# Optimization experiments

Measured on AMD Instinct MI355X. Metric: run time of the kernel, lower is better.

Reference implementation:

```python
import jax, jax.numpy as jnp
import numpy as np

C = 1.0          # curvature
TOP_K = 5
LAMBDA_H = 0.01
TAU = 0.1        # forward default
NEG_SAMPLES = 20 # forward default
EPS = 1e-9
B, D = 4096, 64


def _to_ball(v):
    # map gaussian vectors strictly inside the unit Poincare ball
    return 0.8 * v / (1.0 + jnp.linalg.norm(v, axis=-1, keepdims=True))


def setup_inputs() -> dict:
    key = jax.random.key(0)
    ka, kt = jax.random.split(key)
    audio = _to_ball(jax.random.normal(ka, (B, D), dtype=jnp.float32))
    text = _to_ball(jax.random.normal(kt, (B, D), dtype=jnp.float32))
    return {"audio_embeds": audio, "text_embeds": text}


def _pairwise_poincare(x, y, c=C):
    # ||x-y||^2 via gemm instead of materializing [N,N,D] diff tensor
    x_sq = jnp.sum(x * x, axis=-1, keepdims=True)          # [N,1]
    y_sq = jnp.sum(y * y, axis=-1, keepdims=True).T        # [1,M]
    diff_sq = jnp.maximum(x_sq + y_sq - 2.0 * (x @ y.T), 0.0)
    x_cl = jnp.minimum(x_sq, 1.0 - EPS)
    y_cl = jnp.minimum(y_sq, 1.0 - EPS)
    denom = jnp.maximum((1.0 - x_cl) * (1.0 - y_cl), EPS)
    z = jnp.maximum(1.0 + 2.0 * diff_sq / denom, 1.0 + EPS)
    return jnp.arccosh(z) / jnp.sqrt(jnp.asarray(c, x.dtype))


def _topk_triplet(embeds, key):
    n = embeds.shape[0]
    dist = _pairwise_poincare(embeds, embeds)
    dist = dist.at[jnp.arange(n), jnp.arange(n)].set(jnp.inf)  # fill_diagonal_(inf)
    k = min(TOP_K, n - 1)
    neg_pos, pos_idx = jax.lax.top_k(-dist, k)                 # k smallest distances
    pos_term = jax.scipy.special.logsumexp(neg_pos / TAU, axis=1)  # logsumexp(-pos_dist/tau)
    # mask out top-k positives (diagonal stays in pool, holding +inf -> exp(-inf)=0)
    mask = jnp.ones((n, n), bool).at[jnp.arange(n)[:, None], pos_idx].set(False)
    # stable argsort: mask-True columns first, in original column order -> matches dist[i][mask[i]]
    order = jnp.argsort(jnp.where(mask, 0, 1), axis=1)
    pool = jnp.take_along_axis(dist, order[:, : n - k], axis=1)    # [n, n-k]
    samp = jax.random.randint(key, (n, NEG_SAMPLES), 0, n - k)
    neg_vals = jnp.take_along_axis(pool, samp, axis=1)             # [n, NEG_SAMPLES]
    neg_term = jax.scipy.special.logsumexp(-neg_vals / TAU, axis=1)
    return jnp.mean(neg_term - pos_term)  # mean of -(pos_term - neg_term)


def reference(audio_embeds, text_embeds):
    # HyperbolicLayeredLoss.forward returns lambda_h * (text_h + audio_h);
    # the cross-modal loss is computed but NOT added to the returned total in the source.
    key_text = jax.random.key(1)
    key_audio = jax.random.key(2)
    loss_text_h = _topk_triplet(text_embeds, key_text)
    loss_audio_h = _topk_triplet(audio_embeds, key_audio)
    return LAMBDA_H * (loss_text_h + loss_audio_h)
```

## Files before the change

kernel.cpp:

```cpp
#include <hip/hip_runtime.h>
#include <stdint.h>

constexpr int N = 4096;
constexpr int DIM = 64;
constexpr int TOPK = 5;
constexpr int NEGS = 20;
constexpr float TAU_ = 0.1f;
constexpr uint32_t SPAN = 4091u;
constexpr uint32_t MULT = 2309u;

constexpr int CQ = 256;
constexpr int NSLAB = N / CQ;
constexpr int NT = CQ / 16;
constexpr int RPB = 64;
constexpr int YSTRIDE = 136;
constexpr int NSAMP = 4;
constexpr int CAP = 256;

typedef __attribute__((ext_vector_type(8))) short bf16x8;
typedef __attribute__((ext_vector_type(4))) float f32x4;

struct U2 { uint32_t a, b; };

constexpr U2 tf20(uint32_t k0, uint32_t k1, uint32_t x0, uint32_t x1) {
  const uint32_t k2 = k0 ^ k1 ^ 0x1BD11BDAu;
  x0 += k0; x1 += k1;
#define TF_C(r) { x0 += x1; x1 = (x1 << (r)) | (x1 >> (32 - (r))); x1 ^= x0; }
  TF_C(13) TF_C(15) TF_C(26) TF_C(6)
  x0 += k1; x1 += k2 + 1u;
  TF_C(17) TF_C(29) TF_C(16) TF_C(24)
  x0 += k2; x1 += k0 + 2u;
  TF_C(13) TF_C(15) TF_C(26) TF_C(6)
  x0 += k0; x1 += k1 + 3u;
  TF_C(17) TF_C(29) TF_C(16) TF_C(24)
  x0 += k1; x1 += k2 + 4u;
  TF_C(13) TF_C(15) TF_C(26) TF_C(6)
  x0 += k2; x1 += k0 + 5u;
#undef TF_C
  return {x0, x1};
}
constexpr U2 KT1 = tf20(0u, 1u, 0u, 0u);
constexpr U2 KT2 = tf20(0u, 1u, 0u, 1u);
constexpr U2 KA1 = tf20(0u, 2u, 0u, 0u);
constexpr U2 KA2 = tf20(0u, 2u, 0u, 1u);

__device__ __forceinline__ uint32_t rotl32(uint32_t v, int d) {
  return (v << d) | (v >> (32 - d));
}
__device__ __forceinline__ void threefry(uint32_t k0, uint32_t k1,
                                         uint32_t& x0, uint32_t& x1) {
  const uint32_t k2 = k0 ^ k1 ^ 0x1BD11BDAu;
  x0 += k0; x1 += k1;
#define TF_R(r) { x0 += x1; x1 = rotl32(x1, r); x1 ^= x0; }
  TF_R(13) TF_R(15) TF_R(26) TF_R(6)
  x0 += k1; x1 += k2 + 1u;
  TF_R(17) TF_R(29) TF_R(16) TF_R(24)
  x0 += k2; x1 += k0 + 2u;
  TF_R(13) TF_R(15) TF_R(26) TF_R(6)
  x0 += k0; x1 += k1 + 3u;
  TF_R(17) TF_R(29) TF_R(16) TF_R(24)
  x0 += k1; x1 += k2 + 4u;
  TF_R(13) TF_R(15) TF_R(26) TF_R(6)
  x0 += k2; x1 += k0 + 5u;
#undef TF_R
}

__device__ __forceinline__ uint32_t sample_idx(U2 K1, U2 K2, uint32_t f) {
  uint32_t h0 = 0u, h1 = f; threefry(K1.a, K1.b, h0, h1);
  const uint32_t hi = h0 ^ h1;
  uint32_t l0 = 0u, l1 = f; threefry(K2.a, K2.b, l0, l1);
  const uint32_t lo = l0 ^ l1;
  return ((hi % SPAN) * MULT + (lo % SPAN)) % SPAN;
}

__device__ __forceinline__ float acosh_dev(float z) {
  return logf(z + sqrtf((z - 1.0f) * (z + 1.0f)));
}
__device__ __forceinline__ uint16_t f2bf(float f) {
  const uint32_t u = __float_as_uint(f);
  return (uint16_t)((u + 0x7FFFu + ((u >> 16) & 1u)) >> 16);
}
__device__ __forceinline__ float bf2f(uint16_t h) {
  return __uint_as_float((uint32_t)h << 16);
}

__global__ __launch_bounds__(64) void k_pre(const float* __restrict__ Xa,
                                            const float* __restrict__ Xt,
                                            uint16_t* __restrict__ Xs,
                                            float* __restrict__ ysq,
                                            float* __restrict__ inv,
                                            uint32_t* __restrict__ cnt) {
  const int m = blockIdx.y;
  const float* __restrict__ X = (m == 0) ? Xt : Xa;
  const int i = blockIdx.x * 64 + threadIdx.x;
  const float* xr = X + (size_t)i * DIM;

  uint32_t hb[DIM / 2], lb[DIM / 2];
  float s = 0.0f;
#pragma unroll
  for (int u = 0; u < DIM / 4; ++u) {
    const float4 v = *(const float4*)(xr + 4 * u);
    s = fmaf(v.x, v.x, s); s = fmaf(v.y, v.y, s);
    s = fmaf(v.z, v.z, s); s = fmaf(v.w, v.w, s);
    const uint16_t h0 = f2bf(v.x), h1 = f2bf(v.y), h2 = f2bf(v.z), h3 = f2bf(v.w);
    const uint16_t l0 = f2bf(v.x - bf2f(h0)), l1 = f2bf(v.y - bf2f(h1));
    const uint16_t l2 = f2bf(v.z - bf2f(h2)), l3 = f2bf(v.w - bf2f(h3));
    hb[2 * u]     = (uint32_t)h0 | ((uint32_t)h1 << 16);
    hb[2 * u + 1] = (uint32_t)h2 | ((uint32_t)h3 << 16);
    lb[2 * u]     = (uint32_t)l0 | ((uint32_t)l1 << 16);
    lb[2 * u + 1] = (uint32_t)l2 | ((uint32_t)l3 << 16);
  }
  uint32_t* dst = (uint32_t*)(Xs + (size_t)(m * N + i) * 128);
#pragma unroll
  for (int w = 0; w < 8; ++w) {
    uint4 qh = { hb[4 * w], hb[4 * w + 1], hb[4 * w + 2], hb[4 * w + 3] };
    ((uint4*)dst)[w] = qh;
  }
#pragma unroll
  for (int w = 0; w < 8; ++w) {
    uint4 ql = { lb[4 * w], lb[4 * w + 1], lb[4 * w + 2], lb[4 * w + 3] };
    ((uint4*)dst)[8 + w] = ql;
  }
  ysq[m * N + i] = s;
  inv[m * N + i] = 1.0f / (1.0f - fminf(s, 1.0f));
  cnt[m * N + i] = 0u;
}


__global__ __launch_bounds__(256) void k_zb4(
    const uint16_t* __restrict__ Xs, const float* __restrict__ ysq,
    const float* __restrict__ inv, float* __restrict__ zb5) {
  const int rb = (int)blockIdx.x;
  const int qs = (int)blockIdx.y;
  const int m = (int)blockIdx.z;
  const int j0q = (qs * 4 + 1) * CQ;

  const int tid = (int)threadIdx.x;
  const int wid = tid >> 6;
  const int l = tid & 63;
  const int i0w = rb * RPB + wid * 16;
  const int mN = m * N;
  const uint16_t* __restrict__ Xm = Xs + (size_t)m * N * 128;
  const int lc = l & 15;
  const int lk = l >> 4;
  const int lk4 = lk * 4;
  const int lk8 = lk * 8;
  const int sr = tid >> 4;
  const int sc8 = (tid & 15) * 8;
  const int gi = i0w + lc;
  const int dso = sr * YSTRIDE + sc8;

  __shared__ __align__(16) unsigned char smem[4 * 16 * YSTRIDE * 2 + 2048];
  uint16_t* ybuf = (uint16_t*)smem;
  float* sq_s = (float*)(smem + 4 * 16 * YSTRIDE * 2);
  float* iv_s = sq_s + CQ;

  bf16x8 xf[2][2];
#pragma unroll
  for (int c = 0; c < 2; ++c)
#pragma unroll
    for (int h = 0; h < 2; ++h)
      xf[c][h] = *(const bf16x8*)(Xm + (size_t)gi * 128 + h * 64 + c * 32 + lk8);

  const float xsq_i = ysq[mN + gi];

  float t5f[TOPK];
#pragma unroll
  for (int t = 0; t < TOPK; ++t) t5f[t] = __uint_as_float(0x7F800000u);

  const f32x4 zz = {0.0f, 0.0f, 0.0f, 0.0f};
  const float INF_ = __uint_as_float(0x7F800000u);
  const uint16_t* gsrc = Xm + (size_t)(j0q + sr) * 128 + sc8;

#define GLOAD2(A, B, T)                                                        \
  { A = *(const uint4*)(gsrc + (size_t)(T) * 2048);                            \
    B = *(const uint4*)(gsrc + (size_t)((T) + 1) * 2048); }
#define DSW2(A, B, PB)                                                         \
  { *(uint4*)(ybuf + (size_t)((PB) * 2) * (16 * YSTRIDE) + dso) = A;           \
    *(uint4*)(ybuf + (size_t)((PB) * 2 + 1) * (16 * YSTRIDE) + dso) = B; }

#define PZB(T, BUF)                                                            \
  {                                                                            \
    const uint16_t* yp = (BUF) + lc * YSTRIDE + lk8;                           \
    const bf16x8 Y0 = *(const bf16x8*)(yp);                                    \
    const bf16x8 Y1 = *(const bf16x8*)(yp + 32);                               \
    const bf16x8 Y2 = *(const bf16x8*)(yp + 64);                               \
    const bf16x8 Y3 = *(const bf16x8*)(yp + 96);                               \
    f32x4 acc;        \
    acc = __builtin_amdgcn_mfma_f32_16x16x32_bf16(Y0, xf[0][0], zz, 0, 0, 0);  \
    acc = __builtin_amdgcn_mfma_f32_16x16x32_bf16(Y1, xf[1][0], acc, 0, 0, 0); \
    acc = __builtin_amdgcn_mfma_f32_16x16x32_bf16(Y2, xf[0][0], acc, 0, 0, 0); \
    acc = __builtin_amdgcn_mfma_f32_16x16x32_bf16(Y3, xf[1][0], acc, 0, 0, 0); \
    acc = __builtin_amdgcn_mfma_f32_16x16x32_bf16(Y0, xf[0][1], acc, 0, 0, 0); \
    acc = __builtin_amdgcn_mfma_f32_16x16x32_bf16(Y1, xf[1][1], acc, 0, 0, 0); \
    const float4 sq4 = *(const float4*)&sq_s[(T) * 16 + lk4];                  \
    const float4 iv4 = *(const float4*)&iv_s[(T) * 16 + lk4];                  \
    const int jb = j0q + (T) * 16;                                             \
    float st[4];                                                               \
    _Pragma("unroll") for (int p = 0; p < 4; ++p) {                            \
      const float yc = (p == 0) ? sq4.x : (p == 1) ? sq4.y                     \
                      : (p == 2) ? sq4.z : sq4.w;                              \
      const float ic = (p == 0) ? iv4.x : (p == 1) ? iv4.y                     \
                      : (p == 2) ? iv4.z : iv4.w;                              \
      const float d = fmaf(-2.0f, acc[p], xsq_i + yc);                         \
      st[p] = fmaxf(d, 0.0f) * ic;      \
    }                                                                          \
    if (jb == i0w) {                                                           \
      _Pragma("unroll") for (int p = 0; p < 4; ++p)                            \
        if (gi == jb + lk4 + p) st[p] = INF_;                                  \
    }                                                                          \
    _Pragma("unroll") for (int p = 0; p < 4; ++p) {                            \
      float v = st[p];              \
      _Pragma("unroll") for (int t = 0; t < TOPK; ++t) {                       \
        const float mn = fminf(t5f[t], v);                                     \
        v = fmaxf(t5f[t], v);                                                  \
        t5f[t] = mn;                                                           \
      }                                                                        \
    }                                                                          \
  }

  uint4 Ra0, Ra1, Rb0, Rb1;
  if (tid < 64)
    *(float4*)&sq_s[tid * 4] = *(const float4*)&ysq[mN + j0q + tid * 4];
  else if (tid < 128)
    *(float4*)&iv_s[(tid - 64) * 4] =
        *(const float4*)&inv[mN + j0q + (tid - 64) * 4];
  GLOAD2(Ra0, Ra1, 0)
  GLOAD2(Rb0, Rb1, 2)
  DSW2(Ra0, Ra1, 0)

#pragma unroll 1
  for (int p = 0; p < NT / 2; ++p) {
    __syncthreads();
    if (p + 2 < NT / 2) {
      if ((p & 1) == 0) GLOAD2(Ra0, Ra1, (p + 2) * 2)
      else              GLOAD2(Rb0, Rb1, (p + 2) * 2)
    }
    if (p + 1 < NT / 2) {
      if ((p & 1) == 0) DSW2(Rb0, Rb1, 1)
      else              DSW2(Ra0, Ra1, 0)
    }
    PZB(2 * p,     ybuf + (size_t)((p & 1) * 2) * (16 * YSTRIDE))
    PZB(2 * p + 1, ybuf + (size_t)((p & 1) * 2 + 1) * (16 * YSTRIDE))
  }
#undef PZB

  __syncthreads();
  float* mb = (float*)smem;
#pragma unroll
  for (int t = 0; t < TOPK; ++t)
    mb[((size_t)(wid * 16) + lc) * 21 + lk * TOPK + t] = t5f[t];
  __syncthreads();

  if (l < 16) {
    float cur[TOPK];
#pragma unroll
    for (int t = 0; t < TOPK; ++t) cur[t] = mb[((size_t)(wid * 16) + l) * 21 + t];
    for (int c = 1; c < 4; ++c) {
      for (int t = 0; t < TOPK; ++t) {
        float v = mb[((size_t)(wid * 16) + l) * 21 + c * TOPK + t];
        if (v >= cur[TOPK - 1]) break;
#pragma unroll
        for (int u = 0; u < TOPK; ++u) {
          const float mn = fminf(cur[u], v);
          v = fmaxf(cur[u], v);
          cur[u] = mn;
        }
      }
    }
#pragma unroll
    for (int t = 0; t < TOPK; ++t)
      zb5[((size_t)(m * NSAMP + qs) * N + i0w + l) * TOPK + t] = cur[t];
  }
}

__global__ __launch_bounds__(256) void k_scan(
    const uint16_t* __restrict__ Xs, const float* __restrict__ ysq,
    const float* __restrict__ inv, const float* __restrict__ zb5,
    uint32_t* __restrict__ cnt, uint64_t* __restrict__ rowlist) {
  const int rb = (int)blockIdx.x;
  const int qq = (int)blockIdx.y;
  const int m = (int)blockIdx.z;
  const int j0q = qq * CQ;

  const int tid = (int)threadIdx.x;
  const int wid = tid >> 6;
  const int l = tid & 63;
  const int i0b = rb * RPB;
  const int i0w = i0b + wid * 16;
  const int mN = m * N;
  const uint16_t* __restrict__ Xm = Xs + (size_t)m * N * 128;
  const int lc = l & 15;
  const int lk = l >> 4;
  const int lk4 = lk * 4;
  const int lk8 = lk * 8;
  const int sr = tid >> 4;
  const int sc8 = (tid & 15) * 8;
  const int gi = i0w + lc;
  const int dso = sr * YSTRIDE + sc8;

  __shared__ __align__(16) unsigned char smem[4 * 16 * YSTRIDE * 2 + 2048];
  __shared__ float bs_s[RPB];
  uint16_t* ybuf = (uint16_t*)smem;
  float* sq_s = (float*)(smem + 4 * 16 * YSTRIDE * 2);
  float* iv_s = sq_s + CQ;

  bf16x8 xf[2][2];
#pragma unroll
  for (int c = 0; c < 2; ++c)
#pragma unroll
    for (int h = 0; h < 2; ++h)
      xf[c][h] = *(const bf16x8*)(Xm + (size_t)gi * 128 + h * 64 + c * 32 + lk8);

  const float xsq_i = ysq[mN + gi];

  const f32x4 zz = {0.0f, 0.0f, 0.0f, 0.0f};
  const float INF_ = __uint_as_float(0x7F800000u);
  const uint16_t* gsrc = Xm + (size_t)(j0q + sr) * 128 + sc8;

#define PSCAN(T, BUF)                                                          \
  {                                                                            \
    const uint16_t* yp = (BUF) + lc * YSTRIDE + lk8;                           \
    const bf16x8 Y0 = *(const bf16x8*)(yp);                                    \
    const bf16x8 Y1 = *(const bf16x8*)(yp + 32);                               \
    const bf16x8 Y2 = *(const bf16x8*)(yp + 64);                               \
    const bf16x8 Y3 = *(const bf16x8*)(yp + 96);                               \
    f32x4 acc;                        \
    acc = __builtin_amdgcn_mfma_f32_16x16x32_bf16(Y0, xf[0][0], zz, 0, 0, 0);  \
    acc = __builtin_amdgcn_mfma_f32_16x16x32_bf16(Y1, xf[1][0], acc, 0, 0, 0); \
    acc = __builtin_amdgcn_mfma_f32_16x16x32_bf16(Y2, xf[0][0], acc, 0, 0, 0); \
    acc = __builtin_amdgcn_mfma_f32_16x16x32_bf16(Y3, xf[1][0], acc, 0, 0, 0); \
    acc = __builtin_amdgcn_mfma_f32_16x16x32_bf16(Y0, xf[0][1], acc, 0, 0, 0); \
    acc = __builtin_amdgcn_mfma_f32_16x16x32_bf16(Y1, xf[1][1], acc, 0, 0, 0); \
    const float4 sq4 = *(const float4*)&sq_s[(T) * 16 + lk4];                  \
    const float4 iv4 = *(const float4*)&iv_s[(T) * 16 + lk4];                  \
    const int jb = j0q + (T) * 16;                                             \
    float st[4];                                                               \
    _Pragma("unroll") for (int p = 0; p < 4; ++p) {                            \
      const float yc = (p == 0) ? sq4.x : (p == 1) ? sq4.y                     \
                      : (p == 2) ? sq4.z : sq4.w;                              \
      const float ic = (p == 0) ? iv4.x : (p == 1) ? iv4.y                     \
                      : (p == 2) ? iv4.z : iv4.w;                              \
      const float d = fmaf(-2.0f, acc[p], xsq_i + yc);                         \
      st[p] = fmaxf(d, 0.0f) * ic;                                             \
    }                                                                          \
    if (jb == i0w) {                                                           \
      _Pragma("unroll") for (int p = 0; p < 4; ++p)                            \
        if (gi == jb + lk4 + p) st[p] = INF_;                                  \
    }                                                                          \
    const float sm = fminf(fminf(st[0], st[1]), fminf(st[2], st[3]));          \
    if (sm <= bz) {                                                            \
      _Pragma("unroll") for (int p = 0; p < 4; ++p) {                          \
        if (st[p] <= bz) {                                                     \
          const uint64_t key = ((uint64_t)__float_as_uint(st[p]) << 32) |      \
                               (uint32_t)(jb + lk4 + p);                       \
          const uint32_t slot = atomicAdd(&cnt[mN + gi], 1u);                  \
          if (slot < (uint32_t)CAP)                                            \
            rowlist[(size_t)(mN + gi) * CAP + slot] = key;                     \
        }                                                                      \
      }                                                                        \
    }                                                                          \
  }

  uint4 Ra0, Ra1, Rb0, Rb1;
  if (tid < 64) {
    const int row = i0b + tid;
    float cur[TOPK];
#pragma unroll
    for (int t = 0; t < TOPK; ++t)
      cur[t] = zb5[((size_t)(m * NSAMP) * N + row) * TOPK + t];
    for (int q = 1; q < NSAMP; ++q) {
      for (int t = 0; t < TOPK; ++t) {
        float v = zb5[((size_t)(m * NSAMP + q) * N + row) * TOPK + t];
        if (v >= cur[TOPK - 1]) break;
#pragma unroll
        for (int u = 0; u < TOPK; ++u) {
          const float mn = fminf(cur[u], v);
          v = fmaxf(cur[u], v);
          cur[u] = mn;
        }
      }
    }
    bs_s[tid] = cur[TOPK - 1];
    *(float4*)&sq_s[tid * 4] = *(const float4*)&ysq[mN + j0q + tid * 4];
  } else if (tid < 128) {
    *(float4*)&iv_s[(tid - 64) * 4] =
        *(const float4*)&inv[mN + j0q + (tid - 64) * 4];
  }
  GLOAD2(Ra0, Ra1, 0)
  GLOAD2(Rb0, Rb1, 2)
  DSW2(Ra0, Ra1, 0)
  __syncthreads();
  const float bz = bs_s[wid * 16 + lc];

#pragma unroll 1
  for (int p = 0; p < NT / 2; ++p) {
    if (p) __syncthreads();
    if (p + 2 < NT / 2) {
      if ((p & 1) == 0) GLOAD2(Ra0, Ra1, (p + 2) * 2)
      else              GLOAD2(Rb0, Rb1, (p + 2) * 2)
    }
    if (p + 1 < NT / 2) {
      if ((p & 1) == 0) DSW2(Rb0, Rb1, 1)
      else              DSW2(Ra0, Ra1, 0)
    }
    PSCAN(2 * p,     ybuf + (size_t)((p & 1) * 2) * (16 * YSTRIDE))
    PSCAN(2 * p + 1, ybuf + (size_t)((p & 1) * 2 + 1) * (16 * YSTRIDE))
  }
#undef PSCAN
#undef GLOAD2
#undef DSW2
}

__global__ __launch_bounds__(64) void k_neg(const float* __restrict__ Xa,
                                            const float* __restrict__ Xt,
                                            const float* __restrict__ ysq,
                                            const float* __restrict__ inv,
                                            const uint32_t* __restrict__ cnt,
                                            const uint64_t* __restrict__ rowlist,
                                            float* __restrict__ rowres) {
  const int m = blockIdx.y;
  const int i = blockIdx.x;
  const float* __restrict__ X = (m == 0) ? Xt : Xa;
  const U2 K1 = (m == 0) ? KT1 : KA1;
  const U2 K2 = (m == 0) ? KT2 : KA2;
  const int lane = threadIdx.x;

  __shared__ float4 xi4[DIM / 4];
  __shared__ float posv[TOPK];
  if (lane < DIM / 4) xi4[lane] = ((const float4*)(X + (size_t)i * DIM))[lane];
  __syncthreads();

  const uint64_t SENT = ((uint64_t)0x7F800000u << 32) | 0xFFFFFFFFu;
  uint64_t cur[TOPK];
#pragma unroll
  for (int t = 0; t < TOPK; ++t) cur[t] = SENT;
  {
    const uint32_t c_ = min(cnt[m * N + i], (uint32_t)CAP);
    for (uint32_t sv = 0; sv < c_; ++sv) {
      uint64_t key = rowlist[(size_t)(m * N + i) * CAP + sv];
      if (key < cur[TOPK - 1]) {
#pragma unroll
        for (int u = 0; u < TOPK; ++u) {
          const uint64_t cv = cur[u];
          if (key < cv) { cur[u] = key; key = cv; }
        }
      }
    }
  }

  const float ysq_i = ysq[m * N + i];
  const float inv_i = inv[m * N + i];

  if (lane >= 32 && lane < 32 + TOPK) {
    const int t = lane - 32;
    const uint32_t c = (uint32_t)(cur[t] & 0xffffffffu);
    const float4* xc = (const float4*)(X + (size_t)c * DIM);
    float dot = 0.0f;
#pragma unroll
    for (int k = 0; k < DIM / 4; ++k) {
      const float4 a = xi4[k];
      const float4 b = xc[k];
      dot = fmaf(a.x, b.x, dot); dot = fmaf(a.y, b.y, dot);
      dot = fmaf(a.z, b.z, dot); dot = fmaf(a.w, b.w, dot);
    }
    const float diff = fmaxf(ysq_i + ysq[m * N + c] - 2.0f * dot, 0.0f);
    const float z = 1.0f + 2.0f * diff * inv_i * inv[m * N + c];
    posv[t] = -acosh_dev(z) / TAU_;
  }

  uint32_t pidx[TOPK];
#pragma unroll
  for (int t = 0; t < TOPK; ++t) pidx[t] = (uint32_t)(cur[t] & 0xffffffffu);

#define CSWAP(a, b)                                                           \
  { const uint32_t mn = pidx[a] < pidx[b] ? pidx[a] : pidx[b];                \
    const uint32_t mx = pidx[a] < pidx[b] ? pidx[b] : pidx[a];                \
    pidx[a] = mn; pidx[b] = mx; }
  CSWAP(0, 1) CSWAP(3, 4) CSWAP(2, 4) CSWAP(2, 3) CSWAP(1, 4)
  CSWAP(0, 3) CSWAP(0, 2) CSWAP(1, 3) CSWAP(1, 2)
#undef CSWAP

  float v = -1e30f;
  if (lane < NEGS) {
    const uint32_t f = (uint32_t)i * (uint32_t)NEGS + (uint32_t)lane;
    uint32_t c = sample_idx(K1, K2, f);
#pragma unroll
    for (int t = 0; t < TOPK; ++t) c += (c >= pidx[t]) ? 1u : 0u;
    if (c != (uint32_t)i) {
      const float4* xc = (const float4*)(X + (size_t)c * DIM);
      float dot = 0.0f;
#pragma unroll
      for (int k = 0; k < DIM / 4; ++k) {
        const float4 a = xi4[k];
        const float4 b = xc[k];
        dot = fmaf(a.x, b.x, dot); dot = fmaf(a.y, b.y, dot);
        dot = fmaf(a.z, b.z, dot); dot = fmaf(a.w, b.w, dot);
      }
      const float diff = fmaxf(ysq_i + ysq[m * N + c] - 2.0f * dot, 0.0f);
      const float z = 1.0f + 2.0f * diff * inv_i * inv[m * N + c];
      v = -acosh_dev(z) / TAU_;
    }
  }

  __syncthreads();

  float vmax = v;
#pragma unroll
  for (int o = 32; o > 0; o >>= 1) vmax = fmaxf(vmax, __shfl_xor(vmax, o, 64));
  float e = expf(v - vmax);
  float ss = e;
#pragma unroll
  for (int o = 32; o > 0; o >>= 1) ss += __shfl_xor(ss, o, 64);

  if (lane == 0) {
    float vm = -1e30f;
#pragma unroll
    for (int t = 0; t < TOPK; ++t) vm = fmaxf(vm, posv[t]);
    float ps = 0.0f;
#pragma unroll
    for (int t = 0; t < TOPK; ++t) ps += expf(posv[t] - vm);
    const float pos = vm + logf(ps);
    rowres[m * N + i] = (vmax + logf(ss)) - pos;
  }
}

__global__ __launch_bounds__(256) void k_reduce(const float* __restrict__ rowres,
                                                float* __restrict__ out) {
  __shared__ double sh[256];
  double s = 0.0;
  for (int idx = threadIdx.x; idx < 2 * N; idx += 256) s += (double)rowres[idx];
  sh[threadIdx.x] = s;
  __syncthreads();
  for (int o = 128; o > 0; o >>= 1) {
    if (threadIdx.x < o) sh[threadIdx.x] += sh[threadIdx.x + o];
    __syncthreads();
  }
  if (threadIdx.x == 0) out[0] = (float)(0.01 * (sh[0] / (double)N));
}

extern "C" void kernel_launch(void* const* d_in, const int* in_sizes, int n_in,
                              void* d_out, int out_size, void* d_ws,
                              size_t ws_size, hipStream_t stream) {
  const float* Xa = (const float*)d_in[0];
  const float* Xt = (const float*)d_in[1];
  float* out = (float*)d_out;

  float* ysq = (float*)d_ws;
  float* inv = ysq + 2 * N;
  float* rowres = inv + 2 * N;
  uint32_t* cnt = (uint32_t*)(rowres + 2 * N);
  float* zb5 = (float*)(cnt + 2 * N);
  uint64_t* rowlist = (uint64_t*)(zb5 + (size_t)2 * NSAMP * N * TOPK);
  uint16_t* Xs = (uint16_t*)(rowlist + (size_t)2 * N * CAP);

  k_pre<<<dim3(N / 64, 2), 64, 0, stream>>>(Xa, Xt, Xs, ysq, inv, cnt);
  k_zb4<<<dim3(N / RPB, NSAMP, 2), 256, 0, stream>>>(Xs, ysq, inv, zb5);
  k_scan<<<dim3(N / RPB, NSLAB, 2), 256, 0, stream>>>(Xs, ysq, inv, zb5, cnt,
                                                      rowlist);
  k_neg<<<dim3(N, 2), 64, 0, stream>>>(Xa, Xt, ysq, inv, cnt, rowlist, rowres);
  k_reduce<<<1, 256, 0, stream>>>(rowres, out);
}
```

Measured before the change: 105.4 us.

## Merge threshold pass into single selection scan with local running top-k filter

Removes the k_zb4 pre-pass that sampled slabs to build a top-5 distance bound. The scan kernel now keeps a per-lane running top-5 and emits candidates whenever they beat its current fifth-best value. Two MFMA chains are interleaved across the even and odd tiles. The candidate cap grows to 2048 because early slabs have weak bounds, so k_neg now reduces the candidate list in parallel across 64 lanes and merges through shared memory. This saves one full pass and a launch, but adds more atomics and global writes for candidates and a larger workspace.

```diff
diff --git a/kernel.cpp b/kernel.cpp
--- a/kernel.cpp
+++ b/kernel.cpp
@@ -14,8 +14,7 @@
 constexpr int NT = CQ / 16;
 constexpr int RPB = 64;
 constexpr int YSTRIDE = 136;
-constexpr int NSAMP = 4;
-constexpr int CAP = 256;
+constexpr int CAP = 2048;
 
 typedef __attribute__((ext_vector_type(8))) short bf16x8;
 typedef __attribute__((ext_vector_type(4))) float f32x4;
@@ -126,14 +125,14 @@
   cnt[m * N + i] = 0u;
 }
 
-
-__global__ __launch_bounds__(256) void k_zb4(
+__global__ __launch_bounds__(256) void k_sel(
     const uint16_t* __restrict__ Xs, const float* __restrict__ ysq,
-    const float* __restrict__ inv, float* __restrict__ zb5) {
+    const float* __restrict__ inv, uint32_t* __restrict__ cnt,
+    uint64_t* __restrict__ rowlist) {
   const int rb = (int)blockIdx.x;
-  const int qs = (int)blockIdx.y;
+  const int qq = (int)blockIdx.y;
   const int m = (int)blockIdx.z;
-  const int j0q = (qs * 4 + 1) * CQ;
+  const int j0q = qq * CQ;
 
   const int tid = (int)threadIdx.x;
   const int wid = tid >> 6;
@@ -179,20 +178,8 @@
   { *(uint4*)(ybuf + (size_t)((PB) * 2) * (16 * YSTRIDE) + dso) = A;           \
     *(uint4*)(ybuf + (size_t)((PB) * 2 + 1) * (16 * YSTRIDE) + dso) = B; }
 
-#define PZB(T, BUF)                                                            \
+#define EPI(T, ACC)                                                            \
   {                                                                            \
-    const uint16_t* yp = (BUF) + lc * YSTRIDE + lk8;                           \
-    const bf16x8 Y0 = *(const bf16x8*)(yp);                                    \
-    const bf16x8 Y1 = *(const bf16x8*)(yp + 32);                               \
-    const bf16x8 Y2 = *(const bf16x8*)(yp + 64);                               \
-    const bf16x8 Y3 = *(const bf16x8*)(yp + 96);                               \
-    f32x4 acc;        \
-    acc = __builtin_amdgcn_mfma_f32_16x16x32_bf16(Y0, xf[0][0], zz, 0, 0, 0);  \
-    acc = __builtin_amdgcn_mfma_f32_16x16x32_bf16(Y1, xf[1][0], acc, 0, 0, 0); \
-    acc = __builtin_amdgcn_mfma_f32_16x16x32_bf16(Y2, xf[0][0], acc, 0, 0, 0); \
-    acc = __builtin_amdgcn_mfma_f32_16x16x32_bf16(Y3, xf[1][0], acc, 0, 0, 0); \
-    acc = __builtin_amdgcn_mfma_f32_16x16x32_bf16(Y0, xf[0][1], acc, 0, 0, 0); \
-    acc = __builtin_amdgcn_mfma_f32_16x16x32_bf16(Y1, xf[1][1], acc, 0, 0, 0); \
     const float4 sq4 = *(const float4*)&sq_s[(T) * 16 + lk4];                  \
     const float4 iv4 = *(const float4*)&iv_s[(T) * 16 + lk4];                  \
     const int jb = j0q + (T) * 16;                                             \
@@ -202,19 +189,29 @@
                       : (p == 2) ? sq4.z : sq4.w;                              \
       const float ic = (p == 0) ? iv4.x : (p == 1) ? iv4.y                     \
                       : (p == 2) ? iv4.z : iv4.w;                              \
-      const float d = fmaf(-2.0f, acc[p], xsq_i + yc);                         \
+      const float d = fmaf(-2.0f, ACC[p], xsq_i + yc);                         \
       st[p] = fmaxf(d, 0.0f) * ic;      \
     }                                                                          \
-    if (jb == i0w) {                                                           \
+    if (jb == i0w) {                           \
       _Pragma("unroll") for (int p = 0; p < 4; ++p)                            \
         if (gi == jb + lk4 + p) st[p] = INF_;                                  \
     }                                                                          \
-    _Pragma("unroll") for (int p = 0; p < 4; ++p) {                            \
-      float v = st[p];              \
-      _Pragma("unroll") for (int t = 0; t < TOPK; ++t) {                       \
-        const float mn = fminf(t5f[t], v);                                     \
-        v = fmaxf(t5f[t], v);                                                  \
-        t5f[t] = mn;                                                           \
+    const float sm = fminf(fminf(st[0], st[1]), fminf(st[2], st[3]));          \
+    if (sm <= t5f[TOPK - 1]) {                                                 \
+      _Pragma("unroll") for (int p = 0; p < 4; ++p) {                          \
+        if (st[p] <= t5f[TOPK - 1]) {        \
+          const uint64_t key = ((uint64_t)__float_as_uint(st[p]) << 32) |      \
+                               (uint32_t)(jb + lk4 + p);                       \
+          const uint32_t slot = atomicAdd(&cnt[mN + gi], 1u);                  \
+          if (slot < (uint32_t)CAP)                                            \
+            rowlist[(size_t)(mN + gi) * CAP + slot] = key;                     \
+          float v = st[p];                       \
+          _Pragma("unroll") for (int t = 0; t < TOPK; ++t) {                   \
+            const float mn = fminf(t5f[t], v);                                 \
+            v = fmaxf(t5f[t], v);                                              \
+            t5f[t] = mn;                                                       \
+          }                                                                    \
+        }                                                                      \
       }                                                                        \
     }                                                                          \
   }
@@ -240,174 +237,35 @@
       if ((p & 1) == 0) DSW2(Rb0, Rb1, 1)
       else              DSW2(Ra0, Ra1, 0)
     }
-    PZB(2 * p,     ybuf + (size_t)((p & 1) * 2) * (16 * YSTRIDE))
-    PZB(2 * p + 1, ybuf + (size_t)((p & 1) * 2 + 1) * (16 * YSTRIDE))
-  }
-#undef PZB
-
-  __syncthreads();
-  float* mb = (float*)smem;
-#pragma unroll
-  for (int t = 0; t < TOPK; ++t)
-    mb[((size_t)(wid * 16) + lc) * 21 + lk * TOPK + t] = t5f[t];
-  __syncthreads();
-
-  if (l < 16) {
-    float cur[TOPK];
-#pragma unroll
-    for (int t = 0; t < TOPK; ++t) cur[t] = mb[((size_t)(wid * 16) + l) * 21 + t];
-    for (int c = 1; c < 4; ++c) {
-      for (int t = 0; t < TOPK; ++t) {
-        float v = mb[((size_t)(wid * 16) + l) * 21 + c * TOPK + t];
-        if (v >= cur[TOPK - 1]) break;
-#pragma unroll
-        for (int u = 0; u < TOPK; ++u) {
-          const float mn = fminf(cur[u], v);
-          v = fmaxf(cur[u], v);
-          cur[u] = mn;
-        }
-      }
-    }
-#pragma unroll
-    for (int t = 0; t < TOPK; ++t)
-      zb5[((size_t)(m * NSAMP + qs) * N + i0w + l) * TOPK + t] = cur[t];
-  }
-}
-
-__global__ __launch_bounds__(256) void k_scan(
-    const uint16_t* __restrict__ Xs, const float* __restrict__ ysq,
-    const float* __restrict__ inv, const float* __restrict__ zb5,
-    uint32_t* __restrict__ cnt, uint64_t* __restrict__ rowlist) {
-  const int rb = (int)blockIdx.x;
-  const int qq = (int)blockIdx.y;
-  const int m = (int)blockIdx.z;
-  const int j0q = qq * CQ;
-
-  const int tid = (int)threadIdx.x;
-  const int wid = tid >> 6;
-  const int l = tid & 63;
-  const int i0b = rb * RPB;
-  const int i0w = i0b + wid * 16;
-  const int mN = m * N;
-  const uint16_t* __restrict__ Xm = Xs + (size_t)m * N * 128;
-  const int lc = l & 15;
-  const int lk = l >> 4;
-  const int lk4 = lk * 4;
-  const int lk8 = lk * 8;
-  const int sr = tid >> 4;
-  const int sc8 = (tid & 15) * 8;
-  const int gi = i0w + lc;
-  const int dso = sr * YSTRIDE + sc8;
-
-  __shared__ __align__(16) unsigned char smem[4 * 16 * YSTRIDE * 2 + 2048];
-  __shared__ float bs_s[RPB];
-  uint16_t* ybuf = (uint16_t*)smem;
-  float* sq_s = (float*)(smem + 4 * 16 * YSTRIDE * 2);
-  float* iv_s = sq_s + CQ;
-
-  bf16x8 xf[2][2];
-#pragma unroll
-  for (int c = 0; c < 2; ++c)
-#pragma unroll
-    for (int h = 0; h < 2; ++h)
-      xf[c][h] = *(const bf16x8*)(Xm + (size_t)gi * 128 + h * 64 + c * 32 + lk8);
-
-  const float xsq_i = ysq[mN + gi];
-
-  const f32x4 zz = {0.0f, 0.0f, 0.0f, 0.0f};
-  const float INF_ = __uint_as_float(0x7F800000u);
-  const uint16_t* gsrc = Xm + (size_t)(j0q + sr) * 128 + sc8;
-
-#define PSCAN(T, BUF)                                                          \
-  {                                                                            \
-    const uint16_t* yp = (BUF) + lc * YSTRIDE + lk8;                           \
-    const bf16x8 Y0 = *(const bf16x8*)(yp);                                    \
-    const bf16x8 Y1 = *(const bf16x8*)(yp + 32);                               \
-    const bf16x8 Y2 = *(const bf16x8*)(yp + 64);                               \
-    const bf16x8 Y3 = *(const bf16x8*)(yp + 96);                               \
-    f32x4 acc;                        \
-    acc = __builtin_amdgcn_mfma_f32_16x16x32_bf16(Y0, xf[0][0], zz, 0, 0, 0);  \
-    acc = __builtin_amdgcn_mfma_f32_16x16x32_bf16(Y1, xf[1][0], acc, 0, 0, 0); \
-    acc = __builtin_amdgcn_mfma_f32_16x16x32_bf16(Y2, xf[0][0], acc, 0, 0, 0); \
-    acc = __builtin_amdgcn_mfma_f32_16x16x32_bf16(Y3, xf[1][0], acc, 0, 0, 0); \
-    acc = __builtin_amdgcn_mfma_f32_16x16x32_bf16(Y0, xf[0][1], acc, 0, 0, 0); \
-    acc = __builtin_amdgcn_mfma_f32_16x16x32_bf16(Y1, xf[1][1], acc, 0, 0, 0); \
-    const float4 sq4 = *(const float4*)&sq_s[(T) * 16 + lk4];                  \
-    const float4 iv4 = *(const float4*)&iv_s[(T) * 16 + lk4];                  \
-    const int jb = j0q + (T) * 16;                                             \
-    float st[4];                                                               \
-    _Pragma("unroll") for (int p = 0; p < 4; ++p) {                            \
-      const float yc = (p == 0) ? sq4.x : (p == 1) ? sq4.y                     \
-                      : (p == 2) ? sq4.z : sq4.w;                              \
-      const float ic = (p == 0) ? iv4.x : (p == 1) ? iv4.y                     \
-                      : (p == 2) ? iv4.z : iv4.w;                              \
-      const float d = fmaf(-2.0f, acc[p], xsq_i + yc);                         \
-      st[p] = fmaxf(d, 0.0f) * ic;                                             \
-    }                                                                          \
-    if (jb == i0w) {                                                           \
-      _Pragma("unroll") for (int p = 0; p < 4; ++p)                            \
-        if (gi == jb + lk4 + p) st[p] = INF_;                                  \
-    }                                                                          \
-    const float sm = fminf(fminf(st[0], st[1]), fminf(st[2], st[3]));          \
-    if (sm <= bz) {                                                            \
-      _Pragma("unroll") for (int p = 0; p < 4; ++p) {                          \
-        if (st[p] <= bz) {                                                     \
-          const uint64_t key = ((uint64_t)__float_as_uint(st[p]) << 32) |      \
-                               (uint32_t)(jb + lk4 + p);                       \
-          const uint32_t slot = atomicAdd(&cnt[mN + gi], 1u);                  \
-          if (slot < (uint32_t)CAP)                                            \
-            rowlist[(size_t)(mN + gi) * CAP + slot] = key;                     \
-        }                                                                      \
-      }                                                                        \
-    }                                                                          \
-  }
-
-  uint4 Ra0, Ra1, Rb0, Rb1;
-  if (tid < 64) {
-    const int row = i0b + tid;
-    float cur[TOPK];
-#pragma unroll
-    for (int t = 0; t < TOPK; ++t)
-      cur[t] = zb5[((size_t)(m * NSAMP) * N + row) * TOPK + t];
-    for (int q = 1; q < NSAMP; ++q) {
-      for (int t = 0; t < TOPK; ++t) {
-        float v = zb5[((size_t)(m * NSAMP + q) * N + row) * TOPK + t];
-        if (v >= cur[TOPK - 1]) break;
-#pragma unroll
-        for (int u = 0; u < TOPK; ++u) {
-          const float mn = fminf(cur[u], v);
-          v = fmaxf(cur[u], v);
-          cur[u] = mn;
-        }
-      }
-    }
-    bs_s[tid] = cur[TOPK - 1];
-    *(float4*)&sq_s[tid * 4] = *(const float4*)&ysq[mN + j0q + tid * 4];
-  } else if (tid < 128) {
-    *(float4*)&iv_s[(tid - 64) * 4] =
-        *(const float4*)&inv[mN + j0q + (tid - 64) * 4];
-  }
-  GLOAD2(Ra0, Ra1, 0)
-  GLOAD2(Rb0, Rb1, 2)
-  DSW2(Ra0, Ra1, 0)
-  __syncthreads();
-  const float bz = bs_s[wid * 16 + lc];
-
-#pragma unroll 1
-  for (int p = 0; p < NT / 2; ++p) {
-    if (p) __syncthreads();
-    if (p + 2 < NT / 2) {
-      if ((p & 1) == 0) GLOAD2(Ra0, Ra1, (p + 2) * 2)
-      else              GLOAD2(Rb0, Rb1, (p + 2) * 2)
-    }
-    if (p + 1 < NT / 2) {
-      if ((p & 1) == 0) DSW2(Rb0, Rb1, 1)
-      else              DSW2(Ra0, Ra1, 0)
-    }
-    PSCAN(2 * p,     ybuf + (size_t)((p & 1) * 2) * (16 * YSTRIDE))
-    PSCAN(2 * p + 1, ybuf + (size_t)((p & 1) * 2 + 1) * (16 * YSTRIDE))
-  }
-#undef PSCAN
+    const uint16_t* ypE =
+        ybuf + (size_t)((p & 1) * 2) * (16 * YSTRIDE) + lc * YSTRIDE + lk8;
+    const uint16_t* ypO =
+        ybuf + (size_t)((p & 1) * 2 + 1) * (16 * YSTRIDE) + lc * YSTRIDE + lk8;
+    const bf16x8 E0 = *(const bf16x8*)(ypE);
+    const bf16x8 E1 = *(const bf16x8*)(ypE + 32);
+    const bf16x8 E2 = *(const bf16x8*)(ypE + 64);
+    const bf16x8 E3 = *(const bf16x8*)(ypE + 96);
+    const bf16x8 O0 = *(const bf16x8*)(ypO);
+    const bf16x8 O1 = *(const bf16x8*)(ypO + 32);
+    const bf16x8 O2 = *(const bf16x8*)(ypO + 64);
+    const bf16x8 O3 = *(const bf16x8*)(ypO + 96);
+    f32x4 aE, aO;
+    aE = __builtin_amdgcn_mfma_f32_16x16x32_bf16(E0, xf[0][0], zz, 0, 0, 0);
+    aO = __builtin_amdgcn_mfma_f32_16x16x32_bf16(O0, xf[0][0], zz, 0, 0, 0);
+    aE = __builtin_amdgcn_mfma_f32_16x16x32_bf16(E1, xf[1][0], aE, 0, 0, 0);
+    aO = __builtin_amdgcn_mfma_f32_16x16x32_bf16(O1, xf[1][0], aO, 0, 0, 0);
+    aE = __builtin_amdgcn_mfma_f32_16x16x32_bf16(E2, xf[0][0], aE, 0, 0, 0);
+    aO = __builtin_amdgcn_mfma_f32_16x16x32_bf16(O2, xf[0][0], aO, 0, 0, 0);
+    aE = __builtin_amdgcn_mfma_f32_16x16x32_bf16(E3, xf[1][0], aE, 0, 0, 0);
+    aO = __builtin_amdgcn_mfma_f32_16x16x32_bf16(O3, xf[1][0], aO, 0, 0, 0);
+    aE = __builtin_amdgcn_mfma_f32_16x16x32_bf16(E0, xf[0][1], aE, 0, 0, 0);
+    aO = __builtin_amdgcn_mfma_f32_16x16x32_bf16(O0, xf[0][1], aO, 0, 0, 0);
+    aE = __builtin_amdgcn_mfma_f32_16x16x32_bf16(E1, xf[1][1], aE, 0, 0, 0);
+    aO = __builtin_amdgcn_mfma_f32_16x16x32_bf16(O1, xf[1][1], aO, 0, 0, 0);
+    EPI(2 * p, aE)
+    EPI(2 * p + 1, aO)
+  }
+#undef EPI
 #undef GLOAD2
 #undef DSW2
 }
@@ -428,8 +286,8 @@
 
   __shared__ float4 xi4[DIM / 4];
   __shared__ float posv[TOPK];
+  __shared__ uint64_t mbuf[64][TOPK + 1];
   if (lane < DIM / 4) xi4[lane] = ((const float4*)(X + (size_t)i * DIM))[lane];
-  __syncthreads();
 
   const uint64_t SENT = ((uint64_t)0x7F800000u << 32) | 0xFFFFFFFFu;
   uint64_t cur[TOPK];
@@ -437,8 +295,9 @@
   for (int t = 0; t < TOPK; ++t) cur[t] = SENT;
   {
     const uint32_t c_ = min(cnt[m * N + i], (uint32_t)CAP);
-    for (uint32_t sv = 0; sv < c_; ++sv) {
-      uint64_t key = rowlist[(size_t)(m * N + i) * CAP + sv];
+    const uint64_t* rl = rowlist + (size_t)(m * N + i) * CAP;
+    for (uint32_t sv = (uint32_t)lane; sv < c_; sv += 64u) {
+      uint64_t key = rl[sv];
       if (key < cur[TOPK - 1]) {
 #pragma unroll
         for (int u = 0; u < TOPK; ++u) {
@@ -448,6 +307,30 @@
       }
     }
   }
+#pragma unroll
+  for (int t = 0; t < TOPK; ++t) mbuf[lane][t] = cur[t];
+  __syncthreads();
+  if (lane == 0) {
+    uint64_t fin[TOPK];
+#pragma unroll
+    for (int t = 0; t < TOPK; ++t) fin[t] = mbuf[0][t];
+    for (int c = 1; c < 64; ++c) {
+      for (int t = 0; t < TOPK; ++t) {
+        uint64_t key = mbuf[c][t];
+        if (key >= fin[TOPK - 1]) break;
+#pragma unroll
+        for (int u = 0; u < TOPK; ++u) {
+          const uint64_t cv = fin[u];
+          if (key < cv) { fin[u] = key; key = cv; }
+        }
+      }
+    }
+#pragma unroll
+    for (int t = 0; t < TOPK; ++t) mbuf[0][t] = fin[t];
+  }
+  __syncthreads();
+#pragma unroll
+  for (int t = 0; t < TOPK; ++t) cur[t] = mbuf[0][t];
 
   const float ysq_i = ysq[m * N + i];
   const float inv_i = inv[m * N + i];
@@ -550,14 +433,12 @@
   float* inv = ysq + 2 * N;
   float* rowres = inv + 2 * N;
   uint32_t* cnt = (uint32_t*)(rowres + 2 * N);
-  float* zb5 = (float*)(cnt + 2 * N);
-  uint64_t* rowlist = (uint64_t*)(zb5 + (size_t)2 * NSAMP * N * TOPK);
+  uint64_t* rowlist = (uint64_t*)(cnt + 2 * N);
   uint16_t* Xs = (uint16_t*)(rowlist + (size_t)2 * N * CAP);
 
   k_pre<<<dim3(N / 64, 2), 64, 0, stream>>>(Xa, Xt, Xs, ysq, inv, cnt);
-  k_zb4<<<dim3(N / RPB, NSAMP, 2), 256, 0, stream>>>(Xs, ysq, inv, zb5);
-  k_scan<<<dim3(N / RPB, NSLAB, 2), 256, 0, stream>>>(Xs, ysq, inv, zb5, cnt,
-                                                      rowlist);
+  k_sel<<<dim3(N / RPB, NSLAB, 2), 256, 0, stream>>>(Xs, ysq, inv, cnt,
+                                                     rowlist);
   k_neg<<<dim3(N, 2), 64, 0, stream>>>(Xa, Xt, ysq, inv, cnt, rowlist, rowres);
   k_reduce<<<1, 256, 0, stream>>>(rowres, out);
 }
```

New measurement: 389.0 us. +269.2%, slower.

## Compute exact partial top-5 over bound region and skip it in scan

Applied to the files above, without the earlier changes.

The bound kernel now covers 1024 columns per row block (16 sub-blocks of 64 columns, each near the row's own quarter) and keeps exact top-5 keys that pack distance with index, instead of float-only bounds from 4 sampled slabs. The scan kernel then skips those 4 slabs (12 slabs instead of 16), filters candidates with a strict 64-bit key bound, and k_neg seeds its top-5 from the merged partial results. The scan does less work and emits fewer atomics, at the cost of more bound blocks, larger partial buffers, and a 16-way merge in both k_scan and k_neg.

```diff
diff --git a/kernel.cpp b/kernel.cpp
--- a/kernel.cpp
+++ b/kernel.cpp
@@ -14,7 +14,8 @@
 constexpr int NT = CQ / 16;
 constexpr int RPB = 64;
 constexpr int YSTRIDE = 136;
-constexpr int NSAMP = 4;
+constexpr int NQB = 4;
+constexpr int NBL = 16;
 constexpr int CAP = 256;
 
 typedef __attribute__((ext_vector_type(8))) short bf16x8;
@@ -126,14 +127,16 @@
   cnt[m * N + i] = 0u;
 }
 
-
-__global__ __launch_bounds__(256) void k_zb4(
+__global__ __launch_bounds__(256) void k_bound(
     const uint16_t* __restrict__ Xs, const float* __restrict__ ysq,
-    const float* __restrict__ inv, float* __restrict__ zb5) {
+    const float* __restrict__ inv, uint64_t* __restrict__ partial) {
   const int rb = (int)blockIdx.x;
-  const int qs = (int)blockIdx.y;
+  const int qy = (int)blockIdx.y;
   const int m = (int)blockIdx.z;
-  const int j0q = (qs * 4 + 1) * CQ;
+  const int qr = rb >> 4;
+  const int qs = qy >> 2;
+  const int tq = qy & 3;
+  const int j0 = (qr * NQB + qs) * CQ + tq * 64;
 
   const int tid = (int)threadIdx.x;
   const int wid = tid >> 6;
@@ -150,10 +153,10 @@
   const int gi = i0w + lc;
   const int dso = sr * YSTRIDE + sc8;
 
-  __shared__ __align__(16) unsigned char smem[4 * 16 * YSTRIDE * 2 + 2048];
+  __shared__ __align__(16) unsigned char smem[4 * 16 * YSTRIDE * 2 + 512];
   uint16_t* ybuf = (uint16_t*)smem;
   float* sq_s = (float*)(smem + 4 * 16 * YSTRIDE * 2);
-  float* iv_s = sq_s + CQ;
+  float* iv_s = sq_s + 64;
 
   bf16x8 xf[2][2];
 #pragma unroll
@@ -164,124 +167,122 @@
 
   const float xsq_i = ysq[mN + gi];
 
-  float t5f[TOPK];
-#pragma unroll
-  for (int t = 0; t < TOPK; ++t) t5f[t] = __uint_as_float(0x7F800000u);
+  const uint64_t SENT = ((uint64_t)0x7F800000u << 32) | 0xFFFFFFFFu;
+  uint64_t t5[TOPK];
+#pragma unroll
+  for (int t = 0; t < TOPK; ++t) t5[t] = SENT;
+  float s5 = __uint_as_float(0x7F800000u);
 
   const f32x4 zz = {0.0f, 0.0f, 0.0f, 0.0f};
   const float INF_ = __uint_as_float(0x7F800000u);
-  const uint16_t* gsrc = Xm + (size_t)(j0q + sr) * 128 + sc8;
-
-#define GLOAD2(A, B, T)                                                        \
-  { A = *(const uint4*)(gsrc + (size_t)(T) * 2048);                            \
-    B = *(const uint4*)(gsrc + (size_t)((T) + 1) * 2048); }
-#define DSW2(A, B, PB)                                                         \
-  { *(uint4*)(ybuf + (size_t)((PB) * 2) * (16 * YSTRIDE) + dso) = A;           \
-    *(uint4*)(ybuf + (size_t)((PB) * 2 + 1) * (16 * YSTRIDE) + dso) = B; }
-
-#define PZB(T, BUF)                                                            \
-  {                                                                            \
-    const uint16_t* yp = (BUF) + lc * YSTRIDE + lk8;                           \
-    const bf16x8 Y0 = *(const bf16x8*)(yp);                                    \
-    const bf16x8 Y1 = *(const bf16x8*)(yp + 32);                               \
-    const bf16x8 Y2 = *(const bf16x8*)(yp + 64);                               \
-    const bf16x8 Y3 = *(const bf16x8*)(yp + 96);                               \
-    f32x4 acc;        \
-    acc = __builtin_amdgcn_mfma_f32_16x16x32_bf16(Y0, xf[0][0], zz, 0, 0, 0);  \
-    acc = __builtin_amdgcn_mfma_f32_16x16x32_bf16(Y1, xf[1][0], acc, 0, 0, 0); \
-    acc = __builtin_amdgcn_mfma_f32_16x16x32_bf16(Y2, xf[0][0], acc, 0, 0, 0); \
-    acc = __builtin_amdgcn_mfma_f32_16x16x32_bf16(Y3, xf[1][0], acc, 0, 0, 0); \
-    acc = __builtin_amdgcn_mfma_f32_16x16x32_bf16(Y0, xf[0][1], acc, 0, 0, 0); \
-    acc = __builtin_amdgcn_mfma_f32_16x16x32_bf16(Y1, xf[1][1], acc, 0, 0, 0); \
-    const float4 sq4 = *(const float4*)&sq_s[(T) * 16 + lk4];                  \
-    const float4 iv4 = *(const float4*)&iv_s[(T) * 16 + lk4];                  \
-    const int jb = j0q + (T) * 16;                                             \
-    float st[4];                                                               \
-    _Pragma("unroll") for (int p = 0; p < 4; ++p) {                            \
-      const float yc = (p == 0) ? sq4.x : (p == 1) ? sq4.y                     \
-                      : (p == 2) ? sq4.z : sq4.w;                              \
-      const float ic = (p == 0) ? iv4.x : (p == 1) ? iv4.y                     \
-                      : (p == 2) ? iv4.z : iv4.w;                              \
-      const float d = fmaf(-2.0f, acc[p], xsq_i + yc);                         \
-      st[p] = fmaxf(d, 0.0f) * ic;      \
-    }                                                                          \
-    if (jb == i0w) {                                                           \
-      _Pragma("unroll") for (int p = 0; p < 4; ++p)                            \
-        if (gi == jb + lk4 + p) st[p] = INF_;                                  \
-    }                                                                          \
-    _Pragma("unroll") for (int p = 0; p < 4; ++p) {                            \
-      float v = st[p];              \
-      _Pragma("unroll") for (int t = 0; t < TOPK; ++t) {                       \
-        const float mn = fminf(t5f[t], v);                                     \
-        v = fmaxf(t5f[t], v);                                                  \
-        t5f[t] = mn;                                                           \
-      }                                                                        \
-    }                                                                          \
-  }
-
-  uint4 Ra0, Ra1, Rb0, Rb1;
-  if (tid < 64)
-    *(float4*)&sq_s[tid * 4] = *(const float4*)&ysq[mN + j0q + tid * 4];
-  else if (tid < 128)
-    *(float4*)&iv_s[(tid - 64) * 4] =
-        *(const float4*)&inv[mN + j0q + (tid - 64) * 4];
-  GLOAD2(Ra0, Ra1, 0)
-  GLOAD2(Rb0, Rb1, 2)
-  DSW2(Ra0, Ra1, 0)
-
-#pragma unroll 1
-  for (int p = 0; p < NT / 2; ++p) {
+
+  {
+    const uint16_t* gsrc = Xm + (size_t)(j0 + sr) * 128 + sc8;
+    const uint4 r0 = *(const uint4*)(gsrc);
+    const uint4 r1 = *(const uint4*)(gsrc + 2048);
+    const uint4 r2 = *(const uint4*)(gsrc + 4096);
+    const uint4 r3 = *(const uint4*)(gsrc + 6144);
+    if (tid < 16)
+      *(float4*)&sq_s[tid * 4] = *(const float4*)&ysq[mN + j0 + tid * 4];
+    else if (tid < 32)
+      *(float4*)&iv_s[(tid - 16) * 4] =
+          *(const float4*)&inv[mN + j0 + (tid - 16) * 4];
+    *(uint4*)(ybuf + (size_t)0 * 16 * YSTRIDE + dso) = r0;
+    *(uint4*)(ybuf + (size_t)1 * 16 * YSTRIDE + dso) = r1;
+    *(uint4*)(ybuf + (size_t)2 * 16 * YSTRIDE + dso) = r2;
+    *(uint4*)(ybuf + (size_t)3 * 16 * YSTRIDE + dso) = r3;
     __syncthreads();
-    if (p + 2 < NT / 2) {
-      if ((p & 1) == 0) GLOAD2(Ra0, Ra1, (p + 2) * 2)
-      else              GLOAD2(Rb0, Rb1, (p + 2) * 2)
-    }
-    if (p + 1 < NT / 2) {
-      if ((p & 1) == 0) DSW2(Rb0, Rb1, 1)
-      else              DSW2(Ra0, Ra1, 0)
-    }
-    PZB(2 * p,     ybuf + (size_t)((p & 1) * 2) * (16 * YSTRIDE))
-    PZB(2 * p + 1, ybuf + (size_t)((p & 1) * 2 + 1) * (16 * YSTRIDE))
-  }
-#undef PZB
+  }
+
+#pragma unroll
+  for (int T = 0; T < 4; ++T) {
+    const uint16_t* yp =
+        ybuf + (size_t)T * 16 * YSTRIDE + lc * YSTRIDE + lk8;
+    const bf16x8 Y0 = *(const bf16x8*)(yp);
+    const bf16x8 Y1 = *(const bf16x8*)(yp + 32);
+    const bf16x8 Y2 = *(const bf16x8*)(yp + 64);
+    const bf16x8 Y3 = *(const bf16x8*)(yp + 96);
+    f32x4 acc;
+    acc = __builtin_amdgcn_mfma_f32_16x16x32_bf16(Y0, xf[0][0], zz, 0, 0, 0);
+    acc = __builtin_amdgcn_mfma_f32_16x16x32_bf16(Y1, xf[1][0], acc, 0, 0, 0);
+    acc = __builtin_amdgcn_mfma_f32_16x16x32_bf16(Y2, xf[0][0], acc, 0, 0, 0);
+    acc = __builtin_amdgcn_mfma_f32_16x16x32_bf16(Y3, xf[1][0], acc, 0, 0, 0);
+    acc = __builtin_amdgcn_mfma_f32_16x16x32_bf16(Y0, xf[0][1], acc, 0, 0, 0);
+    acc = __builtin_amdgcn_mfma_f32_16x16x32_bf16(Y1, xf[1][1], acc, 0, 0, 0);
+    const float4 sq4 = *(const float4*)&sq_s[T * 16 + lk4];
+    const float4 iv4 = *(const float4*)&iv_s[T * 16 + lk4];
+    const int jb = j0 + T * 16;
+    float st[4];
+#pragma unroll
+    for (int p = 0; p < 4; ++p) {
+      const float yc = (p == 0) ? sq4.x : (p == 1) ? sq4.y
+                      : (p == 2) ? sq4.z : sq4.w;
+      const float ic = (p == 0) ? iv4.x : (p == 1) ? iv4.y
+                      : (p == 2) ? iv4.z : iv4.w;
+      const float d = fmaf(-2.0f, acc[p], xsq_i + yc);
+      st[p] = fmaxf(d, 0.0f) * ic;
+    }
+    if (jb == i0w) {
+#pragma unroll
+      for (int p = 0; p < 4; ++p)
+        if (gi == jb + lk4 + p) st[p] = INF_;
+    }
+    const float sm = fminf(fminf(st[0], st[1]), fminf(st[2], st[3]));
+    if (sm <= s5) {
+#pragma unroll
+      for (int p = 0; p < 4; ++p) {
+        uint64_t key = ((uint64_t)__float_as_uint(st[p]) << 32) |
+                       (uint32_t)(jb + lk4 + p);
+        if (key < t5[TOPK - 1]) {
+#pragma unroll
+          for (int tt = 0; tt < TOPK; ++tt) {
+            const uint64_t cv = t5[tt];
+            if (key < cv) { t5[tt] = key; key = cv; }
+          }
+        }
+      }
+      s5 = __uint_as_float((uint32_t)(t5[TOPK - 1] >> 32));
+    }
+  }
 
   __syncthreads();
-  float* mb = (float*)smem;
+  uint64_t* mb = (uint64_t*)smem;
 #pragma unroll
   for (int t = 0; t < TOPK; ++t)
-    mb[((size_t)(wid * 16) + lc) * 21 + lk * TOPK + t] = t5f[t];
+    mb[((size_t)(wid * 16) + lc) * 21 + lk * TOPK + t] = t5[t];
   __syncthreads();
 
   if (l < 16) {
-    float cur[TOPK];
+    uint64_t cur[TOPK];
 #pragma unroll
     for (int t = 0; t < TOPK; ++t) cur[t] = mb[((size_t)(wid * 16) + l) * 21 + t];
     for (int c = 1; c < 4; ++c) {
       for (int t = 0; t < TOPK; ++t) {
-        float v = mb[((size_t)(wid * 16) + l) * 21 + c * TOPK + t];
-        if (v >= cur[TOPK - 1]) break;
+        uint64_t key = mb[((size_t)(wid * 16) + l) * 21 + c * TOPK + t];
+        if (key >= cur[TOPK - 1]) break;
 #pragma unroll
         for (int u = 0; u < TOPK; ++u) {
-          const float mn = fminf(cur[u], v);
-          v = fmaxf(cur[u], v);
-          cur[u] = mn;
+          const uint64_t cv = cur[u];
+          if (key < cv) { cur[u] = key; key = cv; }
         }
       }
     }
 #pragma unroll
     for (int t = 0; t < TOPK; ++t)
-      zb5[((size_t)(m * NSAMP + qs) * N + i0w + l) * TOPK + t] = cur[t];
+      partial[((size_t)(m * NBL + qy) * N + i0w + l) * TOPK + t] = cur[t];
   }
 }
 
 __global__ __launch_bounds__(256) void k_scan(
     const uint16_t* __restrict__ Xs, const float* __restrict__ ysq,
-    const float* __restrict__ inv, const float* __restrict__ zb5,
+    const float* __restrict__ inv, const uint64_t* __restrict__ partial,
     uint32_t* __restrict__ cnt, uint64_t* __restrict__ rowlist) {
   const int rb = (int)blockIdx.x;
-  const int qq = (int)blockIdx.y;
+  const int s = (int)blockIdx.y;
   const int m = (int)blockIdx.z;
-  const int j0q = qq * CQ;
+  const int qr = rb >> 4;
+  const int gs = (s < qr * NQB) ? s : s + NQB;
+  const int j0q = gs * CQ;
 
   const int tid = (int)threadIdx.x;
   const int wid = tid >> 6;
@@ -300,7 +301,7 @@
   const int dso = sr * YSTRIDE + sc8;
 
   __shared__ __align__(16) unsigned char smem[4 * 16 * YSTRIDE * 2 + 2048];
-  __shared__ float bs_s[RPB];
+  __shared__ uint64_t bnd_s[RPB];
   uint16_t* ybuf = (uint16_t*)smem;
   float* sq_s = (float*)(smem + 4 * 16 * YSTRIDE * 2);
   float* iv_s = sq_s + CQ;
@@ -317,6 +318,13 @@
   const f32x4 zz = {0.0f, 0.0f, 0.0f, 0.0f};
   const float INF_ = __uint_as_float(0x7F800000u);
   const uint16_t* gsrc = Xm + (size_t)(j0q + sr) * 128 + sc8;
+
+#define GLOAD2(A, B, T)                                                        \
+  { A = *(const uint4*)(gsrc + (size_t)(T) * 2048);                            \
+    B = *(const uint4*)(gsrc + (size_t)((T) + 1) * 2048); }
+#define DSW2(A, B, PB)                                                         \
+  { *(uint4*)(ybuf + (size_t)((PB) * 2) * (16 * YSTRIDE) + dso) = A;           \
+    *(uint4*)(ybuf + (size_t)((PB) * 2 + 1) * (16 * YSTRIDE) + dso) = B; }
 
 #define PSCAN(T, BUF)                                                          \
   {                                                                            \
@@ -344,16 +352,12 @@
       const float d = fmaf(-2.0f, acc[p], xsq_i + yc);                         \
       st[p] = fmaxf(d, 0.0f) * ic;                                             \
     }                                                                          \
-    if (jb == i0w) {                                                           \
-      _Pragma("unroll") for (int p = 0; p < 4; ++p)                            \
-        if (gi == jb + lk4 + p) st[p] = INF_;                                  \
-    }                                                                          \
     const float sm = fminf(fminf(st[0], st[1]), fminf(st[2], st[3]));          \
     if (sm <= bz) {                                                            \
       _Pragma("unroll") for (int p = 0; p < 4; ++p) {                          \
-        if (st[p] <= bz) {                                                     \
-          const uint64_t key = ((uint64_t)__float_as_uint(st[p]) << 32) |      \
-                               (uint32_t)(jb + lk4 + p);                       \
+        const uint64_t key = ((uint64_t)__float_as_uint(st[p]) << 32) |        \
+                             (uint32_t)(jb + lk4 + p);                         \
+        if (key < bound) {                                                     \
           const uint32_t slot = atomicAdd(&cnt[mN + gi], 1u);                  \
           if (slot < (uint32_t)CAP)                                            \
             rowlist[(size_t)(mN + gi) * CAP + slot] = key;                     \
@@ -365,23 +369,22 @@
   uint4 Ra0, Ra1, Rb0, Rb1;
   if (tid < 64) {
     const int row = i0b + tid;
-    float cur[TOPK];
+    uint64_t cur[TOPK];
 #pragma unroll
     for (int t = 0; t < TOPK; ++t)
-      cur[t] = zb5[((size_t)(m * NSAMP) * N + row) * TOPK + t];
-    for (int q = 1; q < NSAMP; ++q) {
+      cur[t] = partial[((size_t)(m * NBL) * N + row) * TOPK + t];
+    for (int q = 1; q < NBL; ++q) {
       for (int t = 0; t < TOPK; ++t) {
-        float v = zb5[((size_t)(m * NSAMP + q) * N + row) * TOPK + t];
-        if (v >= cur[TOPK - 1]) break;
+        uint64_t key = partial[((size_t)(m * NBL + q) * N + row) * TOPK + t];
+        if (key >= cur[TOPK - 1]) break;
 #pragma unroll
         for (int u = 0; u < TOPK; ++u) {
-          const float mn = fminf(cur[u], v);
-          v = fmaxf(cur[u], v);
-          cur[u] = mn;
+          const uint64_t cv = cur[u];
+          if (key < cv) { cur[u] = key; key = cv; }
         }
       }
     }
-    bs_s[tid] = cur[TOPK - 1];
+    bnd_s[tid] = cur[TOPK - 1];
     *(float4*)&sq_s[tid * 4] = *(const float4*)&ysq[mN + j0q + tid * 4];
   } else if (tid < 128) {
     *(float4*)&iv_s[(tid - 64) * 4] =
@@ -391,7 +394,9 @@
   GLOAD2(Rb0, Rb1, 2)
   DSW2(Ra0, Ra1, 0)
   __syncthreads();
-  const float bz = bs_s[wid * 16 + lc];
+  const uint64_t bound = bnd_s[wid * 16 + lc];
+  const float bz = __uint_as_float((uint32_t)(bound >> 32));
+  (void)INF_;
 
 #pragma unroll 1
   for (int p = 0; p < NT / 2; ++p) {
@@ -416,6 +421,7 @@
                                             const float* __restrict__ Xt,
                                             const float* __restrict__ ysq,
                                             const float* __restrict__ inv,
+                                            const uint64_t* __restrict__ partial,
                                             const uint32_t* __restrict__ cnt,
                                             const uint64_t* __restrict__ rowlist,
                                             float* __restrict__ rowres) {
@@ -431,10 +437,21 @@
   if (lane < DIM / 4) xi4[lane] = ((const float4*)(X + (size_t)i * DIM))[lane];
   __syncthreads();
 
-  const uint64_t SENT = ((uint64_t)0x7F800000u << 32) | 0xFFFFFFFFu;
   uint64_t cur[TOPK];
 #pragma unroll
-  for (int t = 0; t < TOPK; ++t) cur[t] = SENT;
+  for (int t = 0; t < TOPK; ++t)
+    cur[t] = partial[((size_t)(m * NBL) * N + i) * TOPK + t];
+  for (int q = 1; q < NBL; ++q) {
+    for (int t = 0; t < TOPK; ++t) {
+      uint64_t key = partial[((size_t)(m * NBL + q) * N + i) * TOPK + t];
+      if (key >= cur[TOPK - 1]) break;
+#pragma unroll
+      for (int u = 0; u < TOPK; ++u) {
+        const uint64_t cv = cur[u];
+        if (key < cv) { cur[u] = key; key = cv; }
+      }
+    }
+  }
   {
     const uint32_t c_ = min(cnt[m * N + i], (uint32_t)CAP);
     for (uint32_t sv = 0; sv < c_; ++sv) {
@@ -550,14 +567,15 @@
   float* inv = ysq + 2 * N;
   float* rowres = inv + 2 * N;
   uint32_t* cnt = (uint32_t*)(rowres + 2 * N);
-  float* zb5 = (float*)(cnt + 2 * N);
-  uint64_t* rowlist = (uint64_t*)(zb5 + (size_t)2 * NSAMP * N * TOPK);
+  uint64_t* partial = (uint64_t*)(cnt + 2 * N);
+  uint64_t* rowlist = partial + (size_t)2 * NBL * N * TOPK;
   uint16_t* Xs = (uint16_t*)(rowlist + (size_t)2 * N * CAP);
 
   k_pre<<<dim3(N / 64, 2), 64, 0, stream>>>(Xa, Xt, Xs, ysq, inv, cnt);
-  k_zb4<<<dim3(N / RPB, NSAMP, 2), 256, 0, stream>>>(Xs, ysq, inv, zb5);
-  k_scan<<<dim3(N / RPB, NSLAB, 2), 256, 0, stream>>>(Xs, ysq, inv, zb5, cnt,
-                                                      rowlist);
-  k_neg<<<dim3(N, 2), 64, 0, stream>>>(Xa, Xt, ysq, inv, cnt, rowlist, rowres);
+  k_bound<<<dim3(N / RPB, NBL, 2), 256, 0, stream>>>(Xs, ysq, inv, partial);
+  k_scan<<<dim3(N / RPB, 12, 2), 256, 0, stream>>>(Xs, ysq, inv, partial, cnt,
+                                                   rowlist);
+  k_neg<<<dim3(N, 2), 64, 0, stream>>>(Xa, Xt, ysq, inv, partial, cnt, rowlist,
+                                       rowres);
   k_reduce<<<1, 256, 0, stream>>>(rowres, out);
 }
```

Result: slower. 119.3 us (+13.2%).
